# Optimization experiments

Hardware: AMD Instinct MI355X
Metric: run time of the kernel (lower is better)

## Reference

```python
import jax, jax.numpy as jnp
import numpy as np

DIM = 384
H = 6
D = DIM // H
MLP = 4 * DIM
SCALE = D ** -0.5
LN_EPS = 1e-5


def _ln(x, w, b):
    m = jnp.mean(x, axis=-1, keepdims=True)
    v = jnp.mean((x - m) ** 2, axis=-1, keepdims=True)
    return (x - m) * jax.lax.rsqrt(v + LN_EPS) * w + b


def setup_inputs() -> dict:
    key = jax.random.key(0)
    ks = jax.random.split(key, 8)
    B, N = 8, 1024
    x = jax.random.normal(ks[0], (B, N, DIM), dtype=jnp.float32)
    # torch nn.Linear weights are [out, in]
    qkv_w = jax.random.normal(ks[1], (3 * DIM, DIM), dtype=jnp.float32) * (DIM ** -0.5)
    proj_w = jax.random.normal(ks[2], (DIM, DIM), dtype=jnp.float32) * (DIM ** -0.5)
    proj_b = jnp.zeros((DIM,), jnp.float32)
    # L2Q params, 'quadratic' init
    alpha = jnp.full((H, 1, 1), 0.125, jnp.float32)
    beta = jnp.full((H, 1, 1), 0.5, jnp.float32)
    gamma = jnp.zeros((H, 1, 1), jnp.float32)
    ln1_w = jnp.ones((DIM,), jnp.float32)
    ln1_b = jnp.zeros((DIM,), jnp.float32)
    ln2_w = jnp.ones((DIM,), jnp.float32)
    ln2_b = jnp.zeros((DIM,), jnp.float32)
    w1 = jax.random.normal(ks[3], (MLP, DIM), dtype=jnp.float32) * (DIM ** -0.5)
    b1 = jnp.zeros((MLP,), jnp.float32)
    w2 = jax.random.normal(ks[4], (DIM, MLP), dtype=jnp.float32) * (MLP ** -0.5)
    b2 = jnp.zeros((DIM,), jnp.float32)
    return {"x": x, "qkv_w": qkv_w, "proj_w": proj_w, "proj_b": proj_b,
            "alpha": alpha, "beta": beta, "gamma": gamma,
            "ln1_w": ln1_w, "ln1_b": ln1_b, "ln2_w": ln2_w, "ln2_b": ln2_b,
            "w1": w1, "b1": b1, "w2": w2, "b2": b2}


def reference(x, qkv_w, proj_w, proj_b, alpha, beta, gamma,
              ln1_w, ln1_b, ln2_w, ln2_b, w1, b1, w2, b2):
    B, N, C = x.shape
    # --- L2Q attention on LN(x) ---
    h = _ln(x, ln1_w, ln1_b)
    qkv = (h @ qkv_w.T).reshape(B, N, 3, H, D)
    q = qkv[:, :, 0].transpose(0, 2, 1, 3)  # [B,H,N,D]
    k = qkv[:, :, 1].transpose(0, 2, 1, 3)
    v = qkv[:, :, 2].transpose(0, 2, 1, 3)
    logits = jnp.einsum('bhnd,bhmd->bhnm', q, k) * SCALE
    attn = jax.nn.relu(alpha * logits ** 2 + beta * logits + gamma)
    attn = attn / (jnp.sum(attn, axis=-1, keepdims=True) + 1e-6)
    out = jnp.einsum('bhnm,bhmd->bhnd', attn, v)
    out = out.transpose(0, 2, 1, 3).reshape(B, N, C)
    x = x + out @ proj_w.T + proj_b
    # --- MLP on LN(x), exact GELU (torch default) ---
    h2 = _ln(x, ln2_w, ln2_b)
    m = jax.nn.gelu(h2 @ w1.T + b1, approximate=False)
    x = x + m @ w2.T + b2
    return x
```

## Files before the change

### kernel.cpp

```cpp
#include <hip/hip_runtime.h>
#include <hip/hip_bf16.h>
#include <math.h>

#define DIMC 384
#define NH 6
#define HD 64
#define MLPD 1536
#define BS 8
#define SEQ 1024
#define T_TOK (BS*SEQ)
#define TC ((size_t)T_TOK*DIMC)
#define QK_SCALE 0.125f

typedef __bf16 bf16;
typedef bf16 bf16x4 __attribute__((ext_vector_type(4)));
typedef bf16 bf16x8 __attribute__((ext_vector_type(8)));
typedef float floatx4 __attribute__((ext_vector_type(4)));

__device__ __forceinline__ void async_cp16(const void* gsrc, void* ldst) {
    __builtin_amdgcn_global_load_lds(
        (const __attribute__((address_space(1))) unsigned int*)gsrc,
        (__attribute__((address_space(3))) unsigned int*)ldst,
        16, 0, 0);
}

__global__ __launch_bounds__(256)
void prep_kernel(const float* __restrict__ s0, const float* __restrict__ s1,
                 const float* __restrict__ s2, const float* __restrict__ s3,
                 bf16* __restrict__ dst,
                 const float* __restrict__ x, const float* __restrict__ lw,
                 const float* __restrict__ lb, bf16* __restrict__ out) {
    if (blockIdx.x < 1728) {
        int i = blockIdx.x * 256 + threadIdx.x;
        const int n0 = 110592, n1 = 36864, n2 = 147456;
        const float4* src; int j;
        if (i < n0)           { src = (const float4*)s0; j = i; }
        else if (i < n0+n1)   { src = (const float4*)s1; j = i - n0; }
        else if (i < n0+n1+n2){ src = (const float4*)s2; j = i - n0 - n1; }
        else                  { src = (const float4*)s3; j = i - n0 - n1 - n2; }
        float4 v = src[j];
        bf16x4 o; o[0] = (bf16)v.x; o[1] = (bf16)v.y; o[2] = (bf16)v.z; o[3] = (bf16)v.w;
        ((bf16x4*)dst)[i] = o;
    } else {
        int row = (blockIdx.x - 1728) * 4 + (threadIdx.x >> 6);
        int t = threadIdx.x & 63;
        const float* xr = x + (size_t)row * DIMC;
        float vals[6];
        float s = 0.f;
        #pragma unroll
        for (int i = 0; i < 6; i++) { vals[i] = xr[t + i*64]; s += vals[i]; }
        #pragma unroll
        for (int m = 32; m; m >>= 1) s += __shfl_xor(s, m);
        float mean = s * (1.0f / DIMC);
        float sq = 0.f;
        #pragma unroll
        for (int i = 0; i < 6; i++) { float d = vals[i] - mean; sq += d * d; }
        #pragma unroll
        for (int m = 32; m; m >>= 1) sq += __shfl_xor(sq, m);
        float rstd = rsqrtf(sq * (1.0f / DIMC) + 1e-5f);
        bf16* orow = out + (size_t)row * DIMC;
        #pragma unroll
        for (int i = 0; i < 6; i++) {
            int c = t + i*64;
            orow[c] = (bf16)((vals[i] - mean) * rstd * lw[c] + lb[c]);
        }
    }
}

__global__ __launch_bounds__(256)
void ln2_fused(const float* __restrict__ x, const bf16* __restrict__ p0,
               const bf16* __restrict__ p1, const float* __restrict__ pb,
               const float* __restrict__ w, const float* __restrict__ b,
               float* __restrict__ x1, bf16* __restrict__ h) {
    int row = blockIdx.x * 4 + (threadIdx.x >> 6);
    int t = threadIdx.x & 63;
    size_t base = (size_t)row * DIMC;
    float vals[6];
    float s = 0.f;
    #pragma unroll
    for (int i = 0; i < 6; i++) {
        int c = t + i*64;
        float v = x[base + c] + (float)p0[base + c] + (float)p1[base + c] + pb[c];
        vals[i] = v; s += v;
    }
    #pragma unroll
    for (int m = 32; m; m >>= 1) s += __shfl_xor(s, m);
    float mean = s * (1.0f / DIMC);
    float sq = 0.f;
    #pragma unroll
    for (int i = 0; i < 6; i++) { float d = vals[i] - mean; sq += d * d; }
    #pragma unroll
    for (int m = 32; m; m >>= 1) sq += __shfl_xor(sq, m);
    float rstd = rsqrtf(sq * (1.0f / DIMC) + 1e-5f);
    #pragma unroll
    for (int i = 0; i < 6; i++) {
        int c = t + i*64;
        x1[base + c] = vals[i];
        h[base + c] = (bf16)((vals[i] - mean) * rstd * w[c] + b[c]);
    }
}

__global__ __launch_bounds__(256)
void reduce4(float* __restrict__ xo, const bf16* __restrict__ p0, const bf16* __restrict__ p1,
             const bf16* __restrict__ p2, const bf16* __restrict__ p3,
             const float* __restrict__ b2) {
    int i = blockIdx.x * 256 + threadIdx.x;
    float4 v = ((const float4*)xo)[i];
    int c = (i % 96) * 4;
    float4 bb = *(const float4*)(b2 + c);
    bf16x4 a0 = ((const bf16x4*)p0)[i], a1 = ((const bf16x4*)p1)[i];
    bf16x4 a2 = ((const bf16x4*)p2)[i], a3 = ((const bf16x4*)p3)[i];
    v.x += bb.x + (float)a0[0] + (float)a1[0] + (float)a2[0] + (float)a3[0];
    v.y += bb.y + (float)a0[1] + (float)a1[1] + (float)a2[1] + (float)a3[1];
    v.z += bb.z + (float)a0[2] + (float)a1[2] + (float)a2[2] + (float)a3[2];
    v.w += bb.w + (float)a0[3] + (float)a1[3] + (float)a2[3] + (float)a3[3];
    ((float4*)xo)[i] = v;
}

enum { EPI_NONE = 0, EPI_QKV = 1, EPI_GELU = 3 };

template<int EPI, int K, int KS, int NX, typename OutT>
__global__ __launch_bounds__(512)
void gemm_bt(const bf16* __restrict__ A, const bf16* __restrict__ W,
             const float* __restrict__ bias, OutT* out, int M, int N) {
    __shared__ __align__(16) bf16 Ash[2][4096];
    __shared__ __align__(16) bf16 Bsh[2][4096];
    constexpr int KB = K / KS;
    constexpr int NK = KB / 32;
    int L = blockIdx.x;
    int xcd = L & 7, ii = L >> 3;
    int ysub = ii & 7, rest = ii >> 3;
    int bx = rest % NX, bz = rest / NX;
    int by = ysub * 8 + xcd;
    int tid = threadIdx.x;
    int lane = tid & 63, w = tid >> 6;
    int quad = lane >> 4, l16 = lane & 15;
    int wr = w >> 2, wc = w & 3;
    int rbase = by * 128 + wr * 64;
    int cbase = bx * 128 + wc * 32;
    int kbase = bz * KB;
    int c1 = tid;
    const bf16* Ag1 = A + (size_t)(by*128 + (c1 >> 2)) * K + kbase + (c1 & 3) * 8;
    const bf16* Wg1 = W + (size_t)(bx*128 + (c1 >> 2)) * K + kbase + (c1 & 3) * 8;
    bf16* As1 = &Ash[0][c1 * 8];
    bf16* Bs1 = &Bsh[0][c1 * 8];

    int arow = wr * 64;
    int brow = wc * 32;

    async_cp16(Ag1, As1);
    async_cp16(Wg1, Bs1);
    __syncthreads();

    floatx4 acc[4][2] = {};
    int buf = 0;
    #pragma unroll
    for (int kk = 0; kk < NK; kk++) {
        if (kk + 1 < NK) {
            int off = (buf ^ 1) * 4096;
            async_cp16(Ag1 + (kk+1)*32, As1 + off);
            async_cp16(Wg1 + (kk+1)*32, Bs1 + off);
        }
        const bf16* Ab = Ash[buf];
        const bf16* Bb = Bsh[buf];
        bf16x8 a[4], bfr[2];
        #pragma unroll
        for (int tm = 0; tm < 4; tm++)
            a[tm] = *(const bf16x8*)&Ab[(arow + tm*16 + l16) * 32 + quad*8];
        #pragma unroll
        for (int tn = 0; tn < 2; tn++)
            bfr[tn] = *(const bf16x8*)&Bb[(brow + tn*16 + l16) * 32 + quad*8];
        #pragma unroll
        for (int tm = 0; tm < 4; tm++)
            #pragma unroll
            for (int tn = 0; tn < 2; tn++)
                acc[tm][tn] = __builtin_amdgcn_mfma_f32_16x16x32_bf16(a[tm], bfr[tn], acc[tm][tn], 0, 0, 0);
        __syncthreads();
        buf ^= 1;
    }

    #pragma unroll
    for (int tm = 0; tm < 4; tm++)
        #pragma unroll
        for (int tn = 0; tn < 2; tn++) {
            if constexpr (EPI == EPI_QKV) {
                int colb = cbase + tn*16 + l16;
                int which = colb / 384;
                int rowb = rbase + tm*16 + quad*4;
                int bb = rowb >> 10;
                if (which == 2) {
                    int rem = colb - 768;
                    int hh = rem >> 6, d = rem & 63;
                    int n = rowb & 1023;
                    bf16x4 pk;
                    #pragma unroll
                    for (int r = 0; r < 4; r++) pk[r] = (bf16)acc[tm][tn][r];
                    *(bf16x4*)((bf16*)out + 2*TC + (((size_t)(bb*NH + hh) * HD + d) << 10) + n) = pk;
                } else {
                    int rem = colb - which*384;
                    int hh = rem >> 6, d = rem & 63;
                    #pragma unroll
                    for (int r = 0; r < 4; r++) {
                        int n = (rowb & 1023) + r;
                        ((bf16*)out)[(size_t)which*TC + (((size_t)(bb*NH + hh) * SEQ + n) << 6) + d]
                            = (bf16)acc[tm][tn][r];
                    }
                }
            } else if constexpr (EPI == EPI_NONE) {
                OutT* ob = out + (size_t)bz * M * N;
                #pragma unroll
                for (int r = 0; r < 4; r++) {
                    int row = rbase + tm*16 + quad*4 + r;
                    int col = cbase + tn*16 + l16;
                    ob[(size_t)row * N + col] = (OutT)acc[tm][tn][r];
                }
            } else {
                #pragma unroll
                for (int r = 0; r < 4; r++) {
                    int row = rbase + tm*16 + quad*4 + r;
                    int col = cbase + tn*16 + l16;
                    float v = acc[tm][tn][r] + bias[col];
                    v = 0.5f * v * (1.0f + erff(v * 0.70710678118f));
                    out[(size_t)row * N + col] = (OutT)v;
                }
            }
        }
}

__global__ __launch_bounds__(256)
void attn_kernel(const bf16* __restrict__ q, const bf16* __restrict__ k,
                 const bf16* __restrict__ vt, const float* __restrict__ alpha,
                 const float* __restrict__ beta, const float* __restrict__ gamma,
                 bf16* __restrict__ attn_out) {
    __shared__ __align__(16) bf16 smem[2][8192];

    int L = blockIdx.x;
    int xcd = L & 7, slot = L >> 3;
    int qt = slot & 15;
    int bh = xcd + ((slot >> 4) << 3);
    int bb = bh / NH, h = bh % NH;
    int q0 = qt * 64;
    int tid = threadIdx.x;
    int w = tid >> 6, lane = tid & 63, quad = lane >> 4, l16 = lane & 15;
    float av = alpha[h] * (QK_SCALE * QK_SCALE), bv = beta[h] * QK_SCALE, gv = gamma[h];
    const bf16* qb  = q  + (size_t)bh * SEQ * HD;
    const bf16* kb  = k  + (size_t)bh * SEQ * HD;
    const bf16* vtb = vt + (size_t)bh * HD * SEQ;

    bf16x8 qa[2];
    #pragma unroll
    for (int s = 0; s < 2; s++)
        qa[s] = *(const bf16x8*)(qb + (size_t)(q0 + w*16 + l16) * HD + s*32 + quad*8);

    floatx4 o[4] = {};
    float rsp = 0.f;
    int krow0 = ((l16 >> 2) << 3) + (l16 & 3);

    #define STAGE(CK, BUF)                                                              \
        {                                                                               \
            bf16* Kb_ = smem[BUF];                                                      \
            bf16* Vb_ = smem[BUF] + 4096;                                               \
            _Pragma("unroll")                                                           \
            for (int call = 0; call < 2; call++) {                                      \
                int i2 = call*256 + tid;                                                \
                int r_ = i2 >> 3, c_ = i2 & 7;                                          \
                int kk_ = (r_ & 3) | (((r_ >> 4) & 1) << 2);                            \
                async_cp16(kb  + (size_t)((CK) + r_) * HD + ((c_ ^ kk_) << 3),          \
                           Kb_ + i2*8);                                                 \
                async_cp16(vtb + (size_t)r_ * SEQ + (CK) + ((c_ ^ (r_ & 7)) << 3),      \
                           Vb_ + i2*8);                                                 \
            }                                                                           \
        }

    STAGE(0, 0);
    __syncthreads();

    for (int c = 0; c < 16; c++) {
        int cur = c & 1;
        if (c < 15) STAGE((c+1)*64, cur ^ 1);
        const bf16* Kb = smem[cur];
        const bf16* Vb = smem[cur] + 4096;
        floatx4 sb[2][2] = {};
        #pragma unroll
        for (int s = 0; s < 2; s++)
            #pragma unroll
            for (int b = 0; b < 2; b++)
                #pragma unroll
                for (int j = 0; j < 2; j++) {
                    int g = b*32 + j*4 + krow0;
                    int kk = (g & 3) | (((g >> 4) & 1) << 2);
                    bf16x8 kf = *(const bf16x8*)(Kb + g*64 + (((s*4 + quad) ^ kk) << 3));
                    sb[b][j] = __builtin_amdgcn_mfma_f32_16x16x32_bf16(kf, qa[s], sb[b][j], 0, 0, 0);
                }
        bf16x8 pf[2];
        #pragma unroll
        for (int b = 0; b < 2; b++)
            #pragma unroll
            for (int j = 0; j < 2; j++)
                #pragma unroll
                for (int r = 0; r < 4; r++) {
                    float xx = sb[b][j][r];
                    float p = fmaxf((av*xx + bv)*xx + gv, 0.f);
                    rsp += p;
                    pf[b][j*4 + r] = (bf16)p;
                }
        #pragma unroll
        for (int b = 0; b < 2; b++)
            #pragma unroll
            for (int d = 0; d < 4; d++) {
                int dr = d*16 + l16;
                bf16x8 vf = *(const bf16x8*)(Vb + dr*64 + ((((b<<2) + quad) ^ (dr & 7)) << 3));
                o[d] = __builtin_amdgcn_mfma_f32_16x16x32_bf16(pf[b], vf, o[d], 0, 0, 0);
            }
        if (c < 15) __syncthreads();
    }

    rsp += __shfl_xor(rsp, 16);
    rsp += __shfl_xor(rsp, 32);
    float rsd[4];
    #pragma unroll
    for (int r = 0; r < 4; r++)
        rsd[r] = __shfl(rsp, quad*4 + r) + 1e-6f;
    #pragma unroll
    for (int d = 0; d < 4; d++)
        #pragma unroll
        for (int r = 0; r < 4; r++) {
            int n = q0 + w*16 + quad*4 + r;
            attn_out[((size_t)(bb*SEQ + n)) * DIMC + h*HD + d*16 + l16] =
                (bf16)(o[d][r] / rsd[r]);
        }
    #undef STAGE
}

extern "C" void kernel_launch(void* const* d_in, const int* in_sizes, int n_in,
                              void* d_out, int out_size, void* d_ws, size_t ws_size,
                              hipStream_t stream) {
    const float* x      = (const float*)d_in[0];
    const float* qkv_w  = (const float*)d_in[1];
    const float* proj_w = (const float*)d_in[2];
    const float* proj_b = (const float*)d_in[3];
    const float* alpha  = (const float*)d_in[4];
    const float* beta   = (const float*)d_in[5];
    const float* gamma  = (const float*)d_in[6];
    const float* ln1_w  = (const float*)d_in[7];
    const float* ln1_b  = (const float*)d_in[8];
    const float* ln2_w  = (const float*)d_in[9];
    const float* ln2_b  = (const float*)d_in[10];
    const float* w1     = (const float*)d_in[11];
    const float* b1     = (const float*)d_in[12];
    const float* w2     = (const float*)d_in[13];
    const float* b2     = (const float*)d_in[14];
    float* out = (float*)d_out;

    char* base = (char*)d_ws;
    bf16* wq_bf = (bf16*)base;
    bf16* wp_bf = wq_bf + 442368;
    bf16* w1_bf = wq_bf + 589824;
    bf16* w2_bf = wq_bf + 1179648;
    bf16* h      = (bf16*)(base + 3538944);
    bf16* qkv    = (bf16*)(base + 9830400);
    bf16* attn_o = (bf16*)(base + 28704768);
    bf16* m      = qkv;
    bf16* Pp     = (bf16*)(base + 34996224);
    bf16* Pm     = (bf16*)(base + 34996224);

    prep_kernel<<<1728 + T_TOK/4, 256, 0, stream>>>(
        qkv_w, proj_w, w1, w2, wq_bf, x, ln1_w, ln1_b, h);
    gemm_bt<EPI_QKV, 384, 1, 9, bf16><<<64*9, 512, 0, stream>>>(
        h, wq_bf, nullptr, qkv, T_TOK, 1152);
    attn_kernel<<<768, 256, 0, stream>>>(
        qkv, qkv + TC, qkv + 2*TC, alpha, beta, gamma, attn_o);
    gemm_bt<EPI_NONE, 384, 2, 3, bf16><<<64*3*2, 512, 0, stream>>>(
        attn_o, wp_bf, nullptr, Pp, T_TOK, DIMC);
    ln2_fused<<<T_TOK/4, 256, 0, stream>>>(x, Pp, Pp + TC, proj_b, ln2_w, ln2_b, out, h);
    gemm_bt<EPI_GELU, 384, 1, 12, bf16><<<64*12, 512, 0, stream>>>(
        h, w1_bf, b1, m, T_TOK, MLPD);
    gemm_bt<EPI_NONE, 1536, 4, 3, bf16><<<64*3*4, 512, 0, stream>>>(
        m, w2_bf, nullptr, Pm, T_TOK, DIMC);
    reduce4<<<TC/4/256, 256, 0, stream>>>(out, Pm, Pm + TC, Pm + 2*TC, Pm + 3*TC, b2);
}
```

Measured before the change: 198.4 us.

## Replace split-K GEMMs with 64-row tiles and fuse residual add into FC2 epilogue

Adds a TM template parameter so the projection and FC2 GEMMs use 64-row tiles without split-K, giving enough blocks without partial-sum buffers. The FC2 GEMM now adds bias and residual directly into the fp32 output, which removes the reduce4 kernel and the bf16 partial sums. ln2_fused now reads a single partial. The cost is longer K loops per block (FC2 runs 48 iterations) and lower MFMA work per loaded B tile. The loop unroll is also reduced to 2.

```diff
diff --git a/kernel.cpp b/kernel.cpp
--- a/kernel.cpp
+++ b/kernel.cpp
@@ -69,7 +69,7 @@
 
 __global__ __launch_bounds__(256)
 void ln2_fused(const float* __restrict__ x, const bf16* __restrict__ p0,
-               const bf16* __restrict__ p1, const float* __restrict__ pb,
+               const float* __restrict__ pb,
                const float* __restrict__ w, const float* __restrict__ b,
                float* __restrict__ x1, bf16* __restrict__ h) {
     int row = blockIdx.x * 4 + (threadIdx.x >> 6);
@@ -80,7 +80,7 @@
     #pragma unroll
     for (int i = 0; i < 6; i++) {
         int c = t + i*64;
-        float v = x[base + c] + (float)p0[base + c] + (float)p1[base + c] + pb[c];
+        float v = x[base + c] + (float)p0[base + c] + pb[c];
         vals[i] = v; s += v;
     }
     #pragma unroll
@@ -100,78 +100,63 @@
     }
 }
 
-__global__ __launch_bounds__(256)
-void reduce4(float* __restrict__ xo, const bf16* __restrict__ p0, const bf16* __restrict__ p1,
-             const bf16* __restrict__ p2, const bf16* __restrict__ p3,
-             const float* __restrict__ b2) {
-    int i = blockIdx.x * 256 + threadIdx.x;
-    float4 v = ((const float4*)xo)[i];
-    int c = (i % 96) * 4;
-    float4 bb = *(const float4*)(b2 + c);
-    bf16x4 a0 = ((const bf16x4*)p0)[i], a1 = ((const bf16x4*)p1)[i];
-    bf16x4 a2 = ((const bf16x4*)p2)[i], a3 = ((const bf16x4*)p3)[i];
-    v.x += bb.x + (float)a0[0] + (float)a1[0] + (float)a2[0] + (float)a3[0];
-    v.y += bb.y + (float)a0[1] + (float)a1[1] + (float)a2[1] + (float)a3[1];
-    v.z += bb.z + (float)a0[2] + (float)a1[2] + (float)a2[2] + (float)a3[2];
-    v.w += bb.w + (float)a0[3] + (float)a1[3] + (float)a2[3] + (float)a3[3];
-    ((float4*)xo)[i] = v;
-}
-
-enum { EPI_NONE = 0, EPI_QKV = 1, EPI_GELU = 3 };
-
-template<int EPI, int K, int KS, int NX, typename OutT>
+enum { EPI_NONE = 0, EPI_QKV = 1, EPI_GELU = 3, EPI_RES = 4 };
+
+template<int EPI, int K, int KS, int NX, int TM, typename OutT>
 __global__ __launch_bounds__(512)
 void gemm_bt(const bf16* __restrict__ A, const bf16* __restrict__ W,
              const float* __restrict__ bias, OutT* out, int M, int N) {
-    __shared__ __align__(16) bf16 Ash[2][4096];
+    __shared__ __align__(16) bf16 Ash[2][TM*32];
     __shared__ __align__(16) bf16 Bsh[2][4096];
     constexpr int KB = K / KS;
     constexpr int NK = KB / 32;
+    constexpr int NY8 = 1024 / TM;
+    constexpr int ACC_M = TM / 32;
     int L = blockIdx.x;
     int xcd = L & 7, ii = L >> 3;
-    int ysub = ii & 7, rest = ii >> 3;
+    int ysub = ii % NY8, rest = ii / NY8;
     int bx = rest % NX, bz = rest / NX;
     int by = ysub * 8 + xcd;
     int tid = threadIdx.x;
     int lane = tid & 63, w = tid >> 6;
     int quad = lane >> 4, l16 = lane & 15;
     int wr = w >> 2, wc = w & 3;
-    int rbase = by * 128 + wr * 64;
+    int rbase = by * TM + wr * (TM/2);
     int cbase = bx * 128 + wc * 32;
     int kbase = bz * KB;
-    int c1 = tid;
-    const bf16* Ag1 = A + (size_t)(by*128 + (c1 >> 2)) * K + kbase + (c1 & 3) * 8;
-    const bf16* Wg1 = W + (size_t)(bx*128 + (c1 >> 2)) * K + kbase + (c1 & 3) * 8;
-    bf16* As1 = &Ash[0][c1 * 8];
-    bf16* Bs1 = &Bsh[0][c1 * 8];
-
-    int arow = wr * 64;
+    const bf16* Ag1 = A + (size_t)(by*TM + (tid >> 2)) * K + kbase + (tid & 3) * 8;
+    const bf16* Wg1 = W + (size_t)(bx*128 + (tid >> 2)) * K + kbase + (tid & 3) * 8;
+    bf16* As1 = &Ash[0][tid * 8];
+    bf16* Bs1 = &Bsh[0][tid * 8];
+    constexpr int ACHUNK = TM * 4;
+
+    int arow = wr * (TM/2);
     int brow = wc * 32;
 
-    async_cp16(Ag1, As1);
+    if (TM == 128 || tid < ACHUNK) async_cp16(Ag1, As1);
     async_cp16(Wg1, Bs1);
     __syncthreads();
 
-    floatx4 acc[4][2] = {};
+    floatx4 acc[ACC_M][2] = {};
     int buf = 0;
-    #pragma unroll
+    #pragma unroll 2
     for (int kk = 0; kk < NK; kk++) {
         if (kk + 1 < NK) {
-            int off = (buf ^ 1) * 4096;
-            async_cp16(Ag1 + (kk+1)*32, As1 + off);
-            async_cp16(Wg1 + (kk+1)*32, Bs1 + off);
+            if (TM == 128 || tid < ACHUNK)
+                async_cp16(Ag1 + (kk+1)*32, As1 + (buf ^ 1) * (TM*32));
+            async_cp16(Wg1 + (kk+1)*32, Bs1 + (buf ^ 1) * 4096);
         }
         const bf16* Ab = Ash[buf];
         const bf16* Bb = Bsh[buf];
-        bf16x8 a[4], bfr[2];
-        #pragma unroll
-        for (int tm = 0; tm < 4; tm++)
+        bf16x8 a[ACC_M], bfr[2];
+        #pragma unroll
+        for (int tm = 0; tm < ACC_M; tm++)
             a[tm] = *(const bf16x8*)&Ab[(arow + tm*16 + l16) * 32 + quad*8];
         #pragma unroll
         for (int tn = 0; tn < 2; tn++)
             bfr[tn] = *(const bf16x8*)&Bb[(brow + tn*16 + l16) * 32 + quad*8];
         #pragma unroll
-        for (int tm = 0; tm < 4; tm++)
+        for (int tm = 0; tm < ACC_M; tm++)
             #pragma unroll
             for (int tn = 0; tn < 2; tn++)
                 acc[tm][tn] = __builtin_amdgcn_mfma_f32_16x16x32_bf16(a[tm], bfr[tn], acc[tm][tn], 0, 0, 0);
@@ -180,7 +165,7 @@
     }
 
     #pragma unroll
-    for (int tm = 0; tm < 4; tm++)
+    for (int tm = 0; tm < ACC_M; tm++)
         #pragma unroll
         for (int tn = 0; tn < 2; tn++) {
             if constexpr (EPI == EPI_QKV) {
@@ -214,6 +199,15 @@
                     int col = cbase + tn*16 + l16;
                     ob[(size_t)row * N + col] = (OutT)acc[tm][tn][r];
                 }
+            } else if constexpr (EPI == EPI_RES) {
+                float* ob = (float*)out;
+                #pragma unroll
+                for (int r = 0; r < 4; r++) {
+                    int row = rbase + tm*16 + quad*4 + r;
+                    int col = cbase + tn*16 + l16;
+                    size_t idx = (size_t)row * N + col;
+                    ob[idx] = ob[idx] + bias[col] + acc[tm][tn][r];
+                }
             } else {
                 #pragma unroll
                 for (int r = 0; r < 4; r++) {
@@ -362,20 +356,18 @@
     bf16* attn_o = (bf16*)(base + 28704768);
     bf16* m      = qkv;
     bf16* Pp     = (bf16*)(base + 34996224);
-    bf16* Pm     = (bf16*)(base + 34996224);
 
     prep_kernel<<<1728 + T_TOK/4, 256, 0, stream>>>(
         qkv_w, proj_w, w1, w2, wq_bf, x, ln1_w, ln1_b, h);
-    gemm_bt<EPI_QKV, 384, 1, 9, bf16><<<64*9, 512, 0, stream>>>(
+    gemm_bt<EPI_QKV, 384, 1, 9, 128, bf16><<<64*9, 512, 0, stream>>>(
         h, wq_bf, nullptr, qkv, T_TOK, 1152);
     attn_kernel<<<768, 256, 0, stream>>>(
         qkv, qkv + TC, qkv + 2*TC, alpha, beta, gamma, attn_o);
-    gemm_bt<EPI_NONE, 384, 2, 3, bf16><<<64*3*2, 512, 0, stream>>>(
+    gemm_bt<EPI_NONE, 384, 1, 3, 64, bf16><<<128*3, 512, 0, stream>>>(
         attn_o, wp_bf, nullptr, Pp, T_TOK, DIMC);
-    ln2_fused<<<T_TOK/4, 256, 0, stream>>>(x, Pp, Pp + TC, proj_b, ln2_w, ln2_b, out, h);
-    gemm_bt<EPI_GELU, 384, 1, 12, bf16><<<64*12, 512, 0, stream>>>(
+    ln2_fused<<<T_TOK/4, 256, 0, stream>>>(x, Pp, proj_b, ln2_w, ln2_b, out, h);
+    gemm_bt<EPI_GELU, 384, 1, 12, 128, bf16><<<64*12, 512, 0, stream>>>(
         h, w1_bf, b1, m, T_TOK, MLPD);
-    gemm_bt<EPI_NONE, 1536, 4, 3, bf16><<<64*3*4, 512, 0, stream>>>(
-        m, w2_bf, nullptr, Pm, T_TOK, DIMC);
-    reduce4<<<TC/4/256, 256, 0, stream>>>(out, Pm, Pm + TC, Pm + 2*TC, Pm + 3*TC, b2);
-}
+    gemm_bt<EPI_RES, 1536, 1, 3, 64, float><<<128*3, 512, 0, stream>>>(
+        m, w2_bf, b2, out, T_TOK, DIMC);
+}
```

After: 206.6 us. 4.1% more time.

## Triple-buffer async LDS staging in GEMM and attention kernels

Applied to the files above, without the earlier changes.

Switches the GEMM and attention kernels from double-buffered to triple-buffered async global-to-LDS copies with a prefetch distance of two stages. Each iteration now does one partial vmcnt wait plus barrier, replacing the full syncthreads after compute. The goal is to hide global load latency and cut barrier stalls. The cost is 1.5x LDS per block, which can lower occupancy, and the inline waitcnt counts depend on how many loads each stage issues.

```diff
diff --git a/kernel.cpp b/kernel.cpp
--- a/kernel.cpp
+++ b/kernel.cpp
@@ -123,8 +123,8 @@
 __global__ __launch_bounds__(512)
 void gemm_bt(const bf16* __restrict__ A, const bf16* __restrict__ W,
              const float* __restrict__ bias, OutT* out, int M, int N) {
-    __shared__ __align__(16) bf16 Ash[2][4096];
-    __shared__ __align__(16) bf16 Bsh[2][4096];
+    __shared__ __align__(16) bf16 Ash[3][4096];
+    __shared__ __align__(16) bf16 Bsh[3][4096];
     constexpr int KB = K / KS;
     constexpr int NK = KB / 32;
     int L = blockIdx.x;
@@ -139,30 +139,27 @@
     int rbase = by * 128 + wr * 64;
     int cbase = bx * 128 + wc * 32;
     int kbase = bz * KB;
-    int c1 = tid;
-    const bf16* Ag1 = A + (size_t)(by*128 + (c1 >> 2)) * K + kbase + (c1 & 3) * 8;
-    const bf16* Wg1 = W + (size_t)(bx*128 + (c1 >> 2)) * K + kbase + (c1 & 3) * 8;
-    bf16* As1 = &Ash[0][c1 * 8];
-    bf16* Bs1 = &Bsh[0][c1 * 8];
+    const bf16* Ag1 = A + (size_t)(by*128 + (tid >> 2)) * K + kbase + (tid & 3) * 8;
+    const bf16* Wg1 = W + (size_t)(bx*128 + (tid >> 2)) * K + kbase + (tid & 3) * 8;
 
     int arow = wr * 64;
     int brow = wc * 32;
 
-    async_cp16(Ag1, As1);
-    async_cp16(Wg1, Bs1);
-    __syncthreads();
+    #define GSTAGE(KK, B) { async_cp16(Ag1 + (KK)*32, &Ash[B][tid*8]); \
+                            async_cp16(Wg1 + (KK)*32, &Bsh[B][tid*8]); }
+    GSTAGE(0, 0);
+    GSTAGE(1, 1);
 
     floatx4 acc[4][2] = {};
-    int buf = 0;
-    #pragma unroll
+    #pragma unroll 3
     for (int kk = 0; kk < NK; kk++) {
-        if (kk + 1 < NK) {
-            int off = (buf ^ 1) * 4096;
-            async_cp16(Ag1 + (kk+1)*32, As1 + off);
-            async_cp16(Wg1 + (kk+1)*32, Bs1 + off);
-        }
-        const bf16* Ab = Ash[buf];
-        const bf16* Bb = Bsh[buf];
+        if (kk + 1 < NK)
+            asm volatile("s_waitcnt vmcnt(2)\n\ts_barrier" ::: "memory");
+        else
+            asm volatile("s_waitcnt vmcnt(0)\n\ts_barrier" ::: "memory");
+        if (kk + 2 < NK) GSTAGE(kk+2, (kk+2)%3);
+        const bf16* Ab = Ash[kk%3];
+        const bf16* Bb = Bsh[kk%3];
         bf16x8 a[4], bfr[2];
         #pragma unroll
         for (int tm = 0; tm < 4; tm++)
@@ -175,9 +172,8 @@
             #pragma unroll
             for (int tn = 0; tn < 2; tn++)
                 acc[tm][tn] = __builtin_amdgcn_mfma_f32_16x16x32_bf16(a[tm], bfr[tn], acc[tm][tn], 0, 0, 0);
-        __syncthreads();
-        buf ^= 1;
-    }
+    }
+    #undef GSTAGE
 
     #pragma unroll
     for (int tm = 0; tm < 4; tm++)
@@ -232,7 +228,7 @@
                  const bf16* __restrict__ vt, const float* __restrict__ alpha,
                  const float* __restrict__ beta, const float* __restrict__ gamma,
                  bf16* __restrict__ attn_out) {
-    __shared__ __align__(16) bf16 smem[2][8192];
+    __shared__ __align__(16) bf16 smem[3][8192];
 
     int L = blockIdx.x;
     int xcd = L & 7, slot = L >> 3;
@@ -273,13 +269,16 @@
         }
 
     STAGE(0, 0);
-    __syncthreads();
+    STAGE(64, 1);
 
     for (int c = 0; c < 16; c++) {
-        int cur = c & 1;
-        if (c < 15) STAGE((c+1)*64, cur ^ 1);
-        const bf16* Kb = smem[cur];
-        const bf16* Vb = smem[cur] + 4096;
+        if (c + 1 < 16)
+            asm volatile("s_waitcnt vmcnt(4)\n\ts_barrier" ::: "memory");
+        else
+            asm volatile("s_waitcnt vmcnt(0)\n\ts_barrier" ::: "memory");
+        if (c + 2 < 16) STAGE((c+2)*64, (c+2)%3);
+        const bf16* Kb = smem[c%3];
+        const bf16* Vb = smem[c%3] + 4096;
         floatx4 sb[2][2] = {};
         #pragma unroll
         for (int s = 0; s < 2; s++)
@@ -312,7 +311,6 @@
                 bf16x8 vf = *(const bf16x8*)(Vb + dr*64 + ((((b<<2) + quad) ^ (dr & 7)) << 3));
                 o[d] = __builtin_amdgcn_mfma_f32_16x16x32_bf16(pf[b], vf, o[d], 0, 0, 0);
             }
-        if (c < 15) __syncthreads();
     }
 
     rsp += __shfl_xor(rsp, 16);
```

After: 197.3 us (median of 2 runs). Within noise of the previous version (-0.5%).
